# Kernel optimization log

Hardware: AMD Instinct MI355X
Metric: run time of the kernel (lower is better)

## Reference

```python
import jax, jax.numpy as jnp
import numpy as np

# Static SMPL kinematic tree (24 joints)
PARENTS = [-1, 0, 0, 0, 1, 2, 3, 4, 5, 6, 7, 8, 9, 9, 9, 12, 13, 14, 16, 17, 18, 19, 20, 21]
NJ = 24      # num joints
FS = 6       # local_feature_size
NF = 7       # bone_dim (1) + FS


def _topo_order(parents):
    children = {i: [] for i in range(len(parents))}
    roots = []
    for i, p in enumerate(parents):
        (roots if p == -1 else children[p]).append(i)
    order = []
    queue = roots[:]
    while queue:
        c = queue.pop(0)
        order.append(c)
        queue.extend(sorted(children[c]))
    return order

TOPO = _topo_order(PARENTS)


def setup_inputs() -> dict:
    key = jax.random.key(0)
    ks = jax.random.split(key, 5)
    B = 524288
    x = jax.random.normal(ks[0], (B, NJ, 1), dtype=jnp.float32)
    s = 1.0 / np.sqrt(NF)
    # Stacked per-joint weights. For the root joint, the parent-feature rows of
    # W1 are multiplied by a zero virtual parent feature, which is exactly
    # equivalent to the original Linear(1, 7) root MLP.
    W1 = jax.random.uniform(ks[1], (NJ, NF, NF), jnp.float32, -s, s)
    b1 = jax.random.uniform(ks[2], (NJ, NF), jnp.float32, -s, s)
    W2 = jax.random.uniform(ks[3], (NJ, NF, FS), jnp.float32, -s, s)
    b2 = jax.random.uniform(ks[4], (NJ, FS), jnp.float32, -s, s)
    return {"x": x, "W1": W1, "b1": b1, "W2": W2, "b2": b2}


def reference(x, W1, b1, W2, b2):
    # x: [B, NJ, 1]; sequential propagation over the fixed kinematic tree.
    B = x.shape[0]
    feats = [None] * NJ
    zero_pf = jnp.zeros((B, FS), x.dtype)
    for i in TOPO:
        p = PARENTS[i]
        pf = zero_pf if p == -1 else feats[p]
        inp = jnp.concatenate([x[:, i, :], pf], axis=-1)  # [B, 7]
        h = jax.nn.relu(inp @ W1[i] + b1[i])               # [B, 7]
        feats[i] = jax.nn.relu(h @ W2[i] + b2[i])          # [B, 6]
    return jnp.concatenate(feats, axis=-1)                 # [B, 144]
```

## Files before the change

### kernel.cpp

```cpp
#include <hip/hip_runtime.h>

#define NJ 24
#define NF 7
#define FS 6
#define THREADS 256
#define CUNITS 12
#define PAD 13

typedef float v4f __attribute__((ext_vector_type(4)));

__device__ constexpr int kParents[NJ] = {-1, 0, 0, 0, 1, 2, 3, 4, 5, 6, 7, 8,
                                          9, 9, 9, 12, 13, 14, 16, 17, 18, 19, 20, 21};

#define JOINT(i)                                                              \
    {                                                                         \
        const int p_ = kParents[i];                                           \
        float inp_[NF];                                                       \
        inp_[0] = xr[i];                                                      \
        _Pragma("unroll")                                                     \
        for (int j = 0; j < FS; ++j)                                          \
            inp_[1 + j] = (p_ < 0) ? 0.0f : feats[(p_ < 0) ? 0 : p_][j];      \
        float h_[NF];                                                         \
        _Pragma("unroll")                                                     \
        for (int j = 0; j < NF; ++j) h_[j] = b1[(i) * NF + j];                \
        _Pragma("unroll")                                                     \
        for (int k = 0; k < NF; ++k) {                                        \
            const float a_ = inp_[k];                                         \
            _Pragma("unroll")                                                 \
            for (int j = 0; j < NF; ++j)                                      \
                h_[j] = fmaf(a_, W1[(i) * NF * NF + k * NF + j], h_[j]);      \
        }                                                                     \
        _Pragma("unroll")                                                     \
        for (int j = 0; j < NF; ++j) h_[j] = fmaxf(h_[j], 0.0f);              \
        float f_[FS];                                                         \
        _Pragma("unroll")                                                     \
        for (int j = 0; j < FS; ++j) f_[j] = b2[(i) * FS + j];                \
        _Pragma("unroll")                                                     \
        for (int k = 0; k < NF; ++k) {                                        \
            const float a_ = h_[k];                                           \
            _Pragma("unroll")                                                 \
            for (int j = 0; j < FS; ++j)                                      \
                f_[j] = fmaf(a_, W2[(i) * NF * FS + k * FS + j], f_[j]);      \
        }                                                                     \
        _Pragma("unroll")                                                     \
        for (int j = 0; j < FS; ++j) {                                        \
            f_[j] = fmaxf(f_[j], 0.0f);                                       \
            feats[i][j] = f_[j];                                              \
        }                                                                     \
        if ((i) & 1) {                                                        \
            const int pp_ = ((i) >> 1) & 3;                                   \
            v4f* st_ = myStage + pp_ * 3;                                     \
            st_[0] = (v4f){feats[(i) - 1][0], feats[(i) - 1][1],              \
                           feats[(i) - 1][2], feats[(i) - 1][3]};             \
            st_[1] = (v4f){feats[(i) - 1][4], feats[(i) - 1][5],              \
                           f_[0], f_[1]};                                     \
            st_[2] = (v4f){f_[2], f_[3], f_[4], f_[5]};                       \
        }                                                                     \
    }

#define FLUSH(C, FR)                                                          \
    {                                                                         \
        _Pragma("unroll")                                                     \
        for (int j = 0; j < CUNITS; ++j) {                                    \
            const int G = j * 64 + lane;                                      \
            const int s = G / CUNITS;                                         \
            const int q = G - s * CUNITS;                                     \
            FR[j] = sm[wid][s * PAD + q];                                     \
        }                                                                     \
        _Pragma("unroll")                                                     \
        for (int j = 0; j < CUNITS; ++j)                                      \
            __builtin_nontemporal_store(FR[j], ap[j] + (C) * 12);             \
    }

#define KEEP12(A)                                                             \
    asm volatile("" :: "v"(A[0]), "v"(A[1]), "v"(A[2]), "v"(A[3]),            \
                 "v"(A[4]), "v"(A[5]), "v"(A[6]), "v"(A[7]),                  \
                 "v"(A[8]), "v"(A[9]), "v"(A[10]), "v"(A[11]));

__global__ __launch_bounds__(THREADS, 2) void se1d_kernel(
    const float* __restrict__ x,
    const float* __restrict__ W1,
    const float* __restrict__ b1,
    const float* __restrict__ W2,
    const float* __restrict__ b2,
    float* __restrict__ out, int B)
{
    __shared__ v4f sm[THREADS / 64][64 * PAD];

    const int t    = threadIdx.x;
    const int lane = t & 63;
    const int wid  = t >> 6;
    const int b    = blockIdx.x * THREADS + t;
    const int wb   = blockIdx.x * THREADS + wid * 64;

    v4f* const myStage = &sm[wid][lane * PAD];

    v4f* ap[CUNITS];
    #pragma unroll
    for (int j = 0; j < CUNITS; ++j) {
        const int G = j * 64 + lane;
        const int s = G / CUNITS;
        const int q = G - s * CUNITS;
        ap[j] = reinterpret_cast<v4f*>(out) + (size_t)wb * 36 + s * 36 + q;
    }

    float xr[NJ];
    {
        const v4f* xv = reinterpret_cast<const v4f*>(x + (size_t)b * NJ);
        #pragma unroll
        for (int c = 0; c < NJ / 4; ++c) {
            v4f v = __builtin_nontemporal_load(xv + c);
            xr[c * 4 + 0] = v.x; xr[c * 4 + 1] = v.y;
            xr[c * 4 + 2] = v.z; xr[c * 4 + 3] = v.w;
        }
    }

    float feats[NJ][FS];
    v4f fra[CUNITS], frb[CUNITS];

    JOINT(0) JOINT(1) JOINT(2) JOINT(3) JOINT(4) JOINT(5) JOINT(6) JOINT(7)
    FLUSH(0, fra);
    JOINT(8) JOINT(9) JOINT(10) JOINT(11)
    JOINT(12) JOINT(13) JOINT(14) JOINT(15)
    FLUSH(1, frb);
    JOINT(16) JOINT(17) JOINT(18) JOINT(19)
    JOINT(20) JOINT(21) JOINT(22) JOINT(23)
    FLUSH(2, fra);

    KEEP12(fra);
    KEEP12(frb);
    (void)B;
}

extern "C" void kernel_launch(void* const* d_in, const int* in_sizes, int n_in,
                              void* d_out, int out_size, void* d_ws, size_t ws_size,
                              hipStream_t stream) {
    const float* x  = (const float*)d_in[0];
    const float* W1 = (const float*)d_in[1];
    const float* b1 = (const float*)d_in[2];
    const float* W2 = (const float*)d_in[3];
    const float* b2 = (const float*)d_in[4];
    float* out = (float*)d_out;
    const int B = in_sizes[0] / NJ;
    const int grid = B / THREADS;
    hipLaunchKernelGGL(se1d_kernel, dim3(grid), dim3(THREADS), 0, stream,
                       x, W1, b1, W2, b2, out, B);
}
```

Before: 92.83 us.

## Use 64-thread blocks, stage all outputs in LDS, then flush once

Shrinks blocks to a single wavefront and gives each lane a full 36-vector LDS row, so all 24 joints finish before one contiguous three-pass store. The interleaved flushes after each group of 8 joints, which overlapped stores with compute, are removed, and each pass now writes fully contiguous memory with simpler addressing. In exchange, more LDS is needed per wave (about 37 KB), which may cap occupancy, and output writes no longer overlap compute within a wave.

```diff
diff --git a/kernel.cpp b/kernel.cpp
--- a/kernel.cpp
+++ b/kernel.cpp
@@ -3,9 +3,7 @@
 #define NJ 24
 #define NF 7
 #define FS 6
-#define THREADS 256
-#define CUNITS 12
-#define PAD 13
+#define SROW 37
 
 typedef float v4f __attribute__((ext_vector_type(4)));
 
@@ -48,7 +46,7 @@
             feats[i][j] = f_[j];                                              \
         }                                                                     \
         if ((i) & 1) {                                                        \
-            const int pp_ = ((i) >> 1) & 3;                                   \
+            const int pp_ = (i) >> 1;                              \
             v4f* st_ = myStage + pp_ * 3;                                     \
             st_[0] = (v4f){feats[(i) - 1][0], feats[(i) - 1][1],              \
                            feats[(i) - 1][2], feats[(i) - 1][3]};             \
@@ -58,18 +56,19 @@
         }                                                                     \
     }
 
-#define FLUSH(C, FR)                                                          \
+#define PASS(P, FR)                                                           \
     {                                                                         \
         _Pragma("unroll")                                                     \
-        for (int j = 0; j < CUNITS; ++j) {                                    \
-            const int G = j * 64 + lane;                                      \
-            const int s = G / CUNITS;                                         \
-            const int q = G - s * CUNITS;                                     \
-            FR[j] = sm[wid][s * PAD + q];                                     \
+        for (int j = 0; j < 12; ++j) {                                        \
+            const int G = (P) * 768 + j * 64 + lane;                          \
+            const int s = G / 36;                                             \
+            const int q = G - s * 36;                                         \
+            FR[j] = sm[s * SROW + q];                                         \
         }                                                                     \
         _Pragma("unroll")                                                     \
-        for (int j = 0; j < CUNITS; ++j)                                      \
-            __builtin_nontemporal_store(FR[j], ap[j] + (C) * 12);             \
+        for (int j = 0; j < 12; ++j)                                          \
+            __builtin_nontemporal_store(FR[j],                                \
+                                        outv + (P) * 768 + j * 64 + lane);    \
     }
 
 #define KEEP12(A)                                                             \
@@ -77,7 +76,7 @@
                  "v"(A[4]), "v"(A[5]), "v"(A[6]), "v"(A[7]),                  \
                  "v"(A[8]), "v"(A[9]), "v"(A[10]), "v"(A[11]));
 
-__global__ __launch_bounds__(THREADS, 2) void se1d_kernel(
+__global__ __launch_bounds__(64) void se1d_kernel(
     const float* __restrict__ x,
     const float* __restrict__ W1,
     const float* __restrict__ b1,
@@ -85,24 +84,14 @@
     const float* __restrict__ b2,
     float* __restrict__ out, int B)
 {
-    __shared__ v4f sm[THREADS / 64][64 * PAD];
+    __shared__ v4f sm[64 * SROW];
 
-    const int t    = threadIdx.x;
-    const int lane = t & 63;
-    const int wid  = t >> 6;
-    const int b    = blockIdx.x * THREADS + t;
-    const int wb   = blockIdx.x * THREADS + wid * 64;
+    const int lane = threadIdx.x;
+    const int base = blockIdx.x * 64;
+    const int b    = base + lane;
 
-    v4f* const myStage = &sm[wid][lane * PAD];
-
-    v4f* ap[CUNITS];
-    #pragma unroll
-    for (int j = 0; j < CUNITS; ++j) {
-        const int G = j * 64 + lane;
-        const int s = G / CUNITS;
-        const int q = G - s * CUNITS;
-        ap[j] = reinterpret_cast<v4f*>(out) + (size_t)wb * 36 + s * 36 + q;
-    }
+    v4f* const myStage = &sm[lane * SROW];
+    v4f* const outv = reinterpret_cast<v4f*>(out) + (size_t)base * 36;
 
     float xr[NJ];
     {
@@ -116,16 +105,16 @@
     }
 
     float feats[NJ][FS];
-    v4f fra[CUNITS], frb[CUNITS];
 
-    JOINT(0) JOINT(1) JOINT(2) JOINT(3) JOINT(4) JOINT(5) JOINT(6) JOINT(7)
-    FLUSH(0, fra);
-    JOINT(8) JOINT(9) JOINT(10) JOINT(11)
-    JOINT(12) JOINT(13) JOINT(14) JOINT(15)
-    FLUSH(1, frb);
-    JOINT(16) JOINT(17) JOINT(18) JOINT(19)
-    JOINT(20) JOINT(21) JOINT(22) JOINT(23)
-    FLUSH(2, fra);
+    JOINT(0)  JOINT(1)  JOINT(2)  JOINT(3)  JOINT(4)  JOINT(5)
+    JOINT(6)  JOINT(7)  JOINT(8)  JOINT(9)  JOINT(10) JOINT(11)
+    JOINT(12) JOINT(13) JOINT(14) JOINT(15) JOINT(16) JOINT(17)
+    JOINT(18) JOINT(19) JOINT(20) JOINT(21) JOINT(22) JOINT(23)
+
+    v4f fra[12], frb[12];
+    PASS(0, fra);
+    PASS(1, frb);
+    PASS(2, fra);
 
     KEEP12(fra);
     KEEP12(frb);
@@ -142,7 +131,7 @@
     const float* b2 = (const float*)d_in[4];
     float* out = (float*)d_out;
     const int B = in_sizes[0] / NJ;
-    const int grid = B / THREADS;
-    hipLaunchKernelGGL(se1d_kernel, dim3(grid), dim3(THREADS), 0, stream,
+    const int grid = B / 64;
+    hipLaunchKernelGGL(se1d_kernel, dim3(grid), dim3(64), 0, stream,
                        x, W1, b1, W2, b2, out, B);
 }
```

After: 108.3 us. +16.7%, slower.
